# Kernel optimization log

Measured on AMD Instinct MI355X. Metric: run time of the kernel, lower is better.

Reference implementation:

```python
import jax, jax.numpy as jnp
import numpy as np

NUM_RELS = 1000
NFEATS = 128
RFEATS = 64
B = 32768
P = 1  # norm order


def setup_inputs() -> dict:
    key = jax.random.key(0)
    k1, k2, k3, k4, k5 = jax.random.split(key, 5)
    h_head = jax.random.normal(k1, (B, NFEATS), dtype=jnp.float32)
    h_tail = jax.random.normal(k2, (B, NFEATS), dtype=jnp.float32)
    rels = jax.random.randint(k3, (B,), 0, NUM_RELS, dtype=jnp.int64)
    rel_emb_table = jax.random.normal(k4, (NUM_RELS, RFEATS), dtype=jnp.float32)
    rel_project_table = jax.random.normal(k5, (NUM_RELS, NFEATS * RFEATS), dtype=jnp.float32)
    return {
        "h_head": h_head,
        "h_tail": h_tail,
        "rels": rels,
        "rel_emb_table": rel_emb_table,
        "rel_project_table": rel_project_table,
    }


def reference(h_head, h_tail, rels, rel_emb_table, rel_project_table):
    # per-relation gathers
    h_rel = rel_emb_table[rels]                                    # [B, rfeats]
    proj_rel = rel_project_table[rels].reshape(-1, NFEATS, RFEATS)  # [B, nfeats, rfeats]
    # batched vector-matrix projection of head/tail into relation space
    ph = jnp.einsum("bn,bnr->br", h_head, proj_rel)               # [B, rfeats]
    pt = jnp.einsum("bn,bnr->br", h_tail, proj_rel)               # [B, rfeats]
    diff = ph + h_rel - pt                                         # [B, rfeats]
    # p=1 norm along last dim, negated score
    return -jnp.sum(jnp.abs(diff), axis=-1)                        # [B]
```

## Files before the change

kernel.cpp:

```cpp
#include <hip/hip_runtime.h>


#define NFEATS   128
#define RFEATS   64
#define NUM_RELS 1000
#define STRIDE   128

#define AS_GLOBAL __attribute__((address_space(1)))
#define AS_SHARED __attribute__((address_space(3)))

__global__ void scatter_kernel(const int* __restrict__ rels,
                               int* __restrict__ cursors,
                               int* __restrict__ bucket, int B) {
    int i = blockIdx.x * blockDim.x + threadIdx.x;
    if (i < B) {
        int r = rels[i];
        int s = atomicAdd(&cursors[r], 1);
        if (s < STRIDE) bucket[(r << 7) + s] = i;
    }
}

__global__ __launch_bounds__(512, 8) void transr_main(
    const float* __restrict__ h_head,
    const float* __restrict__ h_tail,
    const float* __restrict__ rel_emb,
    const float* __restrict__ rel_proj,
    const int*   __restrict__ cursors,
    const int*   __restrict__ bucket,
    float* __restrict__ out)
{
    __shared__ float Plds[NFEATS * RFEATS];

    const int r    = blockIdx.x;
    const int tid  = threadIdx.x;
    const int w    = tid >> 6;
    const int lane = tid & 63;

    const float* Psrc = rel_proj + (size_t)r * (NFEATS * RFEATS);
#if __has_builtin(__builtin_amdgcn_global_load_lds)
#pragma unroll
    for (int it = 0; it < 4; ++it) {
        const int off = (it * 512 + tid) * 4;
        __builtin_amdgcn_global_load_lds(
            (const AS_GLOBAL void*)(Psrc + off),
            (AS_SHARED void*)(Plds + off), 16, 0, 0);
    }
#else
#pragma unroll
    for (int it = 0; it < 4; ++it) {
        const int off = (it * 512 + tid) * 4;
        *(float4*)(Plds + off) = *(const float4*)(Psrc + off);
    }
#endif

    int cnt = cursors[r];
    if (cnt > STRIDE) cnt = STRIDE;

    const float ev = rel_emb[(size_t)r * RFEATS + lane];
    const int* buk = bucket + (r << 7);

    int    rowid[4];
    float2 d2[4];
#pragma unroll
    for (int rr = 0; rr < 4; ++rr) {
        const int li = w * 4 + rr;
        rowid[rr] = (li < cnt) ? buk[li] : -1;
        d2[rr] = make_float2(0.f, 0.f);
        if (rowid[rr] >= 0) {
            const float2 a = *(const float2*)(h_head + (size_t)rowid[rr] * NFEATS + lane * 2);
            const float2 b = *(const float2*)(h_tail + (size_t)rowid[rr] * NFEATS + lane * 2);
            d2[rr].x = a.x - b.x;
            d2[rr].y = a.y - b.y;
        }
    }

    __syncthreads();

    for (int base = 0; base < cnt; base += 32) {
        if (base + w * 4 < cnt) {
            float acc0 = 0.f, acc1 = 0.f, acc2 = 0.f, acc3 = 0.f;

#pragma unroll 8
            for (int q = 0; q < 64; ++q) {
                const float p0 = Plds[(2 * q) * RFEATS + lane];
                const float p1 = Plds[(2 * q + 1) * RFEATS + lane];

                float dx, dy;
                dx = __uint_as_float(__builtin_amdgcn_readlane(__float_as_uint(d2[0].x), q));
                dy = __uint_as_float(__builtin_amdgcn_readlane(__float_as_uint(d2[0].y), q));
                acc0 = fmaf(dx, p0, acc0); acc0 = fmaf(dy, p1, acc0);
                dx = __uint_as_float(__builtin_amdgcn_readlane(__float_as_uint(d2[1].x), q));
                dy = __uint_as_float(__builtin_amdgcn_readlane(__float_as_uint(d2[1].y), q));
                acc1 = fmaf(dx, p0, acc1); acc1 = fmaf(dy, p1, acc1);
                dx = __uint_as_float(__builtin_amdgcn_readlane(__float_as_uint(d2[2].x), q));
                dy = __uint_as_float(__builtin_amdgcn_readlane(__float_as_uint(d2[2].y), q));
                acc2 = fmaf(dx, p0, acc2); acc2 = fmaf(dy, p1, acc2);
                dx = __uint_as_float(__builtin_amdgcn_readlane(__float_as_uint(d2[3].x), q));
                dy = __uint_as_float(__builtin_amdgcn_readlane(__float_as_uint(d2[3].y), q));
                acc3 = fmaf(dx, p0, acc3); acc3 = fmaf(dy, p1, acc3);
            }

            float s[4] = { fabsf(acc0 + ev), fabsf(acc1 + ev),
                           fabsf(acc2 + ev), fabsf(acc3 + ev) };
#pragma unroll
            for (int rr = 0; rr < 4; ++rr) {
                float sv = s[rr];
                sv += __shfl_xor(sv, 1);
                sv += __shfl_xor(sv, 2);
                sv += __shfl_xor(sv, 4);
                sv += __shfl_xor(sv, 8);
                sv += __shfl_xor(sv, 16);
                sv += __shfl_xor(sv, 32);
                if (lane == rr && rowid[rr] >= 0) out[rowid[rr]] = -sv;
            }
        }

        const int nbase = base + 32;
        if (nbase < cnt) {
#pragma unroll
            for (int rr = 0; rr < 4; ++rr) {
                const int li = nbase + w * 4 + rr;
                rowid[rr] = (li < cnt) ? buk[li] : -1;
                d2[rr] = make_float2(0.f, 0.f);
                if (rowid[rr] >= 0) {
                    const float2 a = *(const float2*)(h_head + (size_t)rowid[rr] * NFEATS + lane * 2);
                    const float2 b = *(const float2*)(h_tail + (size_t)rowid[rr] * NFEATS + lane * 2);
                    d2[rr].x = a.x - b.x;
                    d2[rr].y = a.y - b.y;
                }
            }
        }
    }
}

extern "C" void kernel_launch(void* const* d_in, const int* in_sizes, int n_in,
                              void* d_out, int out_size, void* d_ws, size_t ws_size,
                              hipStream_t stream) {
    const float* h_head   = (const float*)d_in[0];
    const float* h_tail   = (const float*)d_in[1];
    const int*   rels     = (const int*)d_in[2];
    const float* rel_emb  = (const float*)d_in[3];
    const float* rel_proj = (const float*)d_in[4];
    float* out = (float*)d_out;

    const int B = in_sizes[2];

    int* cursors = (int*)d_ws;
    int* bucket  = cursors + 1024;

    hipMemsetAsync(cursors, 0, 1024 * sizeof(int), stream);
    scatter_kernel<<<(B + 255) / 256, 256, 0, stream>>>(rels, cursors, bucket, B);
    transr_main<<<NUM_RELS, 512, 0, stream>>>(h_head, h_tail, rel_emb, rel_proj,
                                              cursors, bucket, out);
}
```

Measured before the change: 134.9 us.

## Stage head-tail difference in LDS and pipeline projection loads with compute

Each warp now writes its head-minus-tail rows into a shared Dlds buffer instead of broadcasting them with readlane. Each lane computes four output columns from float4 reads of the projection matrix, over a split of the feature dimension, and a two-stage xor shuffle combines the partial sums. The first 32-row chunk waits on the async global-to-LDS loads in four parts with staged vmcnt waits, so computation begins before the whole matrix has arrived. Occupancy is lowered to six blocks to allow the larger LDS footprint. Blocks with no rows now exit early. The row loop that runs past the first chunk writes Dlds again without a barrier, which is safe only because each warp touches only its own rows.

```diff
diff --git a/kernel.cpp b/kernel.cpp
--- a/kernel.cpp
+++ b/kernel.cpp
@@ -20,7 +20,28 @@
     }
 }
 
-__global__ __launch_bounds__(512, 8) void transr_main(
+__device__ __forceinline__ void reduce_store(const float acc[4][4],
+                                             const int rowid[4],
+                                             float4 e4, int lane,
+                                             float* __restrict__ out) {
+#pragma unroll
+    for (int rr = 0; rr < 4; ++rr) {
+        float a0 = acc[rr][0], a1 = acc[rr][1], a2 = acc[rr][2], a3 = acc[rr][3];
+        a0 += __shfl_xor(a0, 20); a0 += __shfl_xor(a0, 40);
+        a1 += __shfl_xor(a1, 20); a1 += __shfl_xor(a1, 40);
+        a2 += __shfl_xor(a2, 20); a2 += __shfl_xor(a2, 40);
+        a3 += __shfl_xor(a3, 20); a3 += __shfl_xor(a3, 40);
+        float sv = fabsf(a0 + e4.x) + fabsf(a1 + e4.y)
+                 + fabsf(a2 + e4.z) + fabsf(a3 + e4.w);
+        sv += __shfl_xor(sv, 1);
+        sv += __shfl_xor(sv, 2);
+        sv += __shfl_xor(sv, 4);
+        sv += __shfl_xor(sv, 8);
+        if (lane == rr && rowid[rr] >= 0) out[rowid[rr]] = -sv;
+    }
+}
+
+__global__ __launch_bounds__(512, 6) void transr_main(
     const float* __restrict__ h_head,
     const float* __restrict__ h_tail,
     const float* __restrict__ rel_emb,
@@ -30,105 +51,124 @@
     float* __restrict__ out)
 {
     __shared__ float Plds[NFEATS * RFEATS];
+    __shared__ float Dlds[32][NFEATS];
 
     const int r    = blockIdx.x;
     const int tid  = threadIdx.x;
     const int w    = tid >> 6;
     const int lane = tid & 63;
+    const int jg   = lane & 15;
+    const int p    = lane >> 4;
+    const int cq   = jg ^ (p << 2);
+
+    int cnt = cursors[r];
+    if (cnt > STRIDE) cnt = STRIDE;
+    if (cnt == 0) return;
+
+    const int* buk = bucket + (r << 7);
+
+    int rowid[4];
+#pragma unroll
+    for (int rr = 0; rr < 4; ++rr) {
+        const int li  = (w << 2) + rr;
+        const int row = (li < cnt) ? buk[li] : -1;
+        rowid[rr] = row;
+        float2 d = make_float2(0.f, 0.f);
+        if (row >= 0) {
+            const float2 a = *(const float2*)(h_head + (size_t)row * NFEATS + (lane << 1));
+            const float2 b = *(const float2*)(h_tail + (size_t)row * NFEATS + (lane << 1));
+            d.x = a.x - b.x;
+            d.y = a.y - b.y;
+        }
+        *(float2*)(&Dlds[(w << 2) + rr][lane << 1]) = d;
+    }
 
     const float* Psrc = rel_proj + (size_t)r * (NFEATS * RFEATS);
-#if __has_builtin(__builtin_amdgcn_global_load_lds)
 #pragma unroll
     for (int it = 0; it < 4; ++it) {
         const int off = (it * 512 + tid) * 4;
-        __builtin_amdgcn_global_load_lds(
-            (const AS_GLOBAL void*)(Psrc + off),
-            (AS_SHARED void*)(Plds + off), 16, 0, 0);
+        __builtin_amdgcn_global_load_lds((const AS_GLOBAL void*)(Psrc + off),
+                                         (AS_SHARED void*)(Plds + off), 16, 0, 0);
     }
-#else
-#pragma unroll
-    for (int it = 0; it < 4; ++it) {
-        const int off = (it * 512 + tid) * 4;
-        *(float4*)(Plds + off) = *(const float4*)(Psrc + off);
-    }
-#endif
+    __builtin_amdgcn_sched_barrier(0);
 
-    int cnt = cursors[r];
-    if (cnt > STRIDE) cnt = STRIDE;
-
-    const float ev = rel_emb[(size_t)r * RFEATS + lane];
-    const int* buk = bucket + (r << 7);
-
-    int    rowid[4];
-    float2 d2[4];
+    float acc[4][4];
 #pragma unroll
     for (int rr = 0; rr < 4; ++rr) {
-        const int li = w * 4 + rr;
-        rowid[rr] = (li < cnt) ? buk[li] : -1;
-        d2[rr] = make_float2(0.f, 0.f);
-        if (rowid[rr] >= 0) {
-            const float2 a = *(const float2*)(h_head + (size_t)rowid[rr] * NFEATS + lane * 2);
-            const float2 b = *(const float2*)(h_tail + (size_t)rowid[rr] * NFEATS + lane * 2);
-            d2[rr].x = a.x - b.x;
-            d2[rr].y = a.y - b.y;
+        acc[rr][0] = 0.f; acc[rr][1] = 0.f; acc[rr][2] = 0.f; acc[rr][3] = 0.f;
+    }
+
+    const char*  Pb   = (const char*)Plds;
+    const int    pcq  = (p << 8) | (cq << 4);
+    const float* drow = &Dlds[w << 2][p];
+    bool havework = ((w << 2) < cnt);
+
+#pragma unroll
+    for (int s = 0; s < 4; ++s) {
+        if      (s == 0) asm volatile("s_waitcnt vmcnt(3)" ::: "memory");
+        else if (s == 1) asm volatile("s_waitcnt vmcnt(2)" ::: "memory");
+        else if (s == 2) asm volatile("s_waitcnt vmcnt(1)" ::: "memory");
+        else             asm volatile("s_waitcnt vmcnt(0)" ::: "memory");
+        __builtin_amdgcn_sched_barrier(0);
+        __builtin_amdgcn_s_barrier();
+        if (havework) {
+#pragma unroll
+            for (int t = 0; t < 8; ++t) {
+                const float4 pv = *(const float4*)(Pb + s * 8192 + t * 1024 + pcq);
+#pragma unroll
+                for (int rr = 0; rr < 4; ++rr) {
+                    const float dv = drow[rr * 128 + s * 32 + t * 4];
+                    acc[rr][0] = fmaf(dv, pv.x, acc[rr][0]);
+                    acc[rr][1] = fmaf(dv, pv.y, acc[rr][1]);
+                    acc[rr][2] = fmaf(dv, pv.z, acc[rr][2]);
+                    acc[rr][3] = fmaf(dv, pv.w, acc[rr][3]);
+                }
+            }
         }
     }
 
-    __syncthreads();
+    const float4 e4 = *(const float4*)(rel_emb + (size_t)r * RFEATS + (cq << 2));
 
-    for (int base = 0; base < cnt; base += 32) {
-        if (base + w * 4 < cnt) {
-            float acc0 = 0.f, acc1 = 0.f, acc2 = 0.f, acc3 = 0.f;
+    if (havework) reduce_store(acc, rowid, e4, lane, out);
 
-#pragma unroll 8
-            for (int q = 0; q < 64; ++q) {
-                const float p0 = Plds[(2 * q) * RFEATS + lane];
-                const float p1 = Plds[(2 * q + 1) * RFEATS + lane];
+    for (int base = 32; base < cnt; base += 32) {
+#pragma unroll
+        for (int rr = 0; rr < 4; ++rr) {
+            const int li  = base + (w << 2) + rr;
+            const int row = (li < cnt) ? buk[li] : -1;
+            rowid[rr] = row;
+            float2 d = make_float2(0.f, 0.f);
+            if (row >= 0) {
+                const float2 a = *(const float2*)(h_head + (size_t)row * NFEATS + (lane << 1));
+                const float2 b = *(const float2*)(h_tail + (size_t)row * NFEATS + (lane << 1));
+                d.x = a.x - b.x;
+                d.y = a.y - b.y;
+            }
+            *(float2*)(&Dlds[(w << 2) + rr][lane << 1]) = d;
+        }
 
-                float dx, dy;
-                dx = __uint_as_float(__builtin_amdgcn_readlane(__float_as_uint(d2[0].x), q));
-                dy = __uint_as_float(__builtin_amdgcn_readlane(__float_as_uint(d2[0].y), q));
-                acc0 = fmaf(dx, p0, acc0); acc0 = fmaf(dy, p1, acc0);
-                dx = __uint_as_float(__builtin_amdgcn_readlane(__float_as_uint(d2[1].x), q));
-                dy = __uint_as_float(__builtin_amdgcn_readlane(__float_as_uint(d2[1].y), q));
-                acc1 = fmaf(dx, p0, acc1); acc1 = fmaf(dy, p1, acc1);
-                dx = __uint_as_float(__builtin_amdgcn_readlane(__float_as_uint(d2[2].x), q));
-                dy = __uint_as_float(__builtin_amdgcn_readlane(__float_as_uint(d2[2].y), q));
-                acc2 = fmaf(dx, p0, acc2); acc2 = fmaf(dy, p1, acc2);
-                dx = __uint_as_float(__builtin_amdgcn_readlane(__float_as_uint(d2[3].x), q));
-                dy = __uint_as_float(__builtin_amdgcn_readlane(__float_as_uint(d2[3].y), q));
-                acc3 = fmaf(dx, p0, acc3); acc3 = fmaf(dy, p1, acc3);
-            }
-
-            float s[4] = { fabsf(acc0 + ev), fabsf(acc1 + ev),
-                           fabsf(acc2 + ev), fabsf(acc3 + ev) };
+        havework = (base + (w << 2) < cnt);
+        if (havework) {
 #pragma unroll
             for (int rr = 0; rr < 4; ++rr) {
-                float sv = s[rr];
-                sv += __shfl_xor(sv, 1);
-                sv += __shfl_xor(sv, 2);
-                sv += __shfl_xor(sv, 4);
-                sv += __shfl_xor(sv, 8);
-                sv += __shfl_xor(sv, 16);
-                sv += __shfl_xor(sv, 32);
-                if (lane == rr && rowid[rr] >= 0) out[rowid[rr]] = -sv;
+                acc[rr][0] = 0.f; acc[rr][1] = 0.f; acc[rr][2] = 0.f; acc[rr][3] = 0.f;
             }
-        }
-
-        const int nbase = base + 32;
-        if (nbase < cnt) {
 #pragma unroll
-            for (int rr = 0; rr < 4; ++rr) {
-                const int li = nbase + w * 4 + rr;
-                rowid[rr] = (li < cnt) ? buk[li] : -1;
-                d2[rr] = make_float2(0.f, 0.f);
-                if (rowid[rr] >= 0) {
-                    const float2 a = *(const float2*)(h_head + (size_t)rowid[rr] * NFEATS + lane * 2);
-                    const float2 b = *(const float2*)(h_tail + (size_t)rowid[rr] * NFEATS + lane * 2);
-                    d2[rr].x = a.x - b.x;
-                    d2[rr].y = a.y - b.y;
+            for (int s = 0; s < 4; ++s) {
+#pragma unroll
+                for (int t = 0; t < 8; ++t) {
+                    const float4 pv = *(const float4*)(Pb + s * 8192 + t * 1024 + pcq);
+#pragma unroll
+                    for (int rr = 0; rr < 4; ++rr) {
+                        const float dv = drow[rr * 128 + s * 32 + t * 4];
+                        acc[rr][0] = fmaf(dv, pv.x, acc[rr][0]);
+                        acc[rr][1] = fmaf(dv, pv.y, acc[rr][1]);
+                        acc[rr][2] = fmaf(dv, pv.z, acc[rr][2]);
+                        acc[rr][3] = fmaf(dv, pv.w, acc[rr][3]);
+                    }
                 }
             }
+            reduce_store(acc, rowid, e4, lane, out);
         }
     }
 }
```

After: 215.2 us. +59.5%, slower.

## Process two relations per block with double-buffered LDS projection staging

Applied to the files above, without the earlier changes.

Each block now handles two relations, using two LDS buffers. The second relation's 32KB projection matrix is loaded asynchronously into LDS while the first relation's rows are computed, which hides global-to-LDS latency. In exchange the grid is halved to 500 blocks and LDS per block doubles to 64KB, which lowers occupancy and parallelism on a GPU with 256 CUs. There is also a possible hazard: the second buffer is written while the first is being read, though the two buffers are separate.

```diff
diff --git a/kernel.cpp b/kernel.cpp
--- a/kernel.cpp
+++ b/kernel.cpp
@@ -20,6 +20,72 @@
     }
 }
 
+
+#define STAGE(PBUF, RIDX)                                                      \
+    {                                                                          \
+        const float* Psrc_ = rel_proj + (size_t)(RIDX) * (NFEATS * RFEATS);    \
+        _Pragma("unroll")                                                      \
+        for (int it_ = 0; it_ < 4; ++it_) {                                    \
+            const int off_ = (it_ * 512 + tid) * 4;                            \
+            __builtin_amdgcn_global_load_lds(                                  \
+                (const AS_GLOBAL void*)(Psrc_ + off_),                         \
+                (AS_SHARED void*)((PBUF) + off_), 16, 0, 0);                   \
+        }                                                                      \
+    }
+
+#define LOADD(CNT, BUK, BASE)                                                  \
+    _Pragma("unroll")                                                          \
+    for (int rr_ = 0; rr_ < 4; ++rr_) {                                        \
+        const int li_ = (BASE) + (w << 2) + rr_;                               \
+        rowid[rr_] = (li_ < (CNT)) ? (BUK)[li_] : -1;                          \
+        d2[rr_] = make_float2(0.f, 0.f);                                       \
+        if (rowid[rr_] >= 0) {                                                 \
+            const float2 a_ = *(const float2*)(h_head + (size_t)rowid[rr_] * NFEATS + (lane << 1)); \
+            const float2 b_ = *(const float2*)(h_tail + (size_t)rowid[rr_] * NFEATS + (lane << 1)); \
+            d2[rr_].x = a_.x - b_.x;                                           \
+            d2[rr_].y = a_.y - b_.y;                                           \
+        }                                                                      \
+    }
+
+#define RL(dst, src, q) dst = __uint_as_float(__builtin_amdgcn_readlane(__float_as_uint(src), q))
+
+#define COMPUTE(CNT, BUK, PBUF, EV)                                            \
+    for (int base_ = 0; base_ < (CNT); base_ += 32) {                          \
+        if (base_ + (w << 2) < (CNT)) {                                        \
+            float acc0 = 0.f, acc1 = 0.f, acc2 = 0.f, acc3 = 0.f;              \
+            _Pragma("unroll 8")                                                \
+            for (int q = 0; q < 64; ++q) {                                     \
+                const float p0 = (PBUF)[(2 * q) * RFEATS + lane];              \
+                const float p1 = (PBUF)[(2 * q + 1) * RFEATS + lane];          \
+                float dx, dy;                                                  \
+                RL(dx, d2[0].x, q); RL(dy, d2[0].y, q);                        \
+                acc0 = fmaf(dx, p0, acc0); acc0 = fmaf(dy, p1, acc0);          \
+                RL(dx, d2[1].x, q); RL(dy, d2[1].y, q);                        \
+                acc1 = fmaf(dx, p0, acc1); acc1 = fmaf(dy, p1, acc1);          \
+                RL(dx, d2[2].x, q); RL(dy, d2[2].y, q);                        \
+                acc2 = fmaf(dx, p0, acc2); acc2 = fmaf(dy, p1, acc2);          \
+                RL(dx, d2[3].x, q); RL(dy, d2[3].y, q);                        \
+                acc3 = fmaf(dx, p0, acc3); acc3 = fmaf(dy, p1, acc3);          \
+            }                                                                  \
+            float s0 = fabsf(acc0 + (EV)), s1 = fabsf(acc1 + (EV));            \
+            float s2 = fabsf(acc2 + (EV)), s3 = fabsf(acc3 + (EV));            \
+            float sv_[4] = { s0, s1, s2, s3 };                                 \
+            _Pragma("unroll")                                                  \
+            for (int rr_ = 0; rr_ < 4; ++rr_) {                                \
+                float sv = sv_[rr_];                                           \
+                sv += __shfl_xor(sv, 1);                                       \
+                sv += __shfl_xor(sv, 2);                                       \
+                sv += __shfl_xor(sv, 4);                                       \
+                sv += __shfl_xor(sv, 8);                                       \
+                sv += __shfl_xor(sv, 16);                                      \
+                sv += __shfl_xor(sv, 32);                                      \
+                if (lane == rr_ && rowid[rr_] >= 0) out[rowid[rr_]] = -sv;     \
+            }                                                                  \
+        }                                                                      \
+        const int nb_ = base_ + 32;                                            \
+        if (nb_ < (CNT)) { LOADD((CNT), (BUK), nb_) }                          \
+    }
+
 __global__ __launch_bounds__(512, 8) void transr_main(
     const float* __restrict__ h_head,
     const float* __restrict__ h_tail,
@@ -29,108 +95,39 @@
     const int*   __restrict__ bucket,
     float* __restrict__ out)
 {
-    __shared__ float Plds[NFEATS * RFEATS];
+    __shared__ float Plds[2][NFEATS * RFEATS];
 
-    const int r    = blockIdx.x;
     const int tid  = threadIdx.x;
     const int w    = tid >> 6;
     const int lane = tid & 63;
 
-    const float* Psrc = rel_proj + (size_t)r * (NFEATS * RFEATS);
-#if __has_builtin(__builtin_amdgcn_global_load_lds)
-#pragma unroll
-    for (int it = 0; it < 4; ++it) {
-        const int off = (it * 512 + tid) * 4;
-        __builtin_amdgcn_global_load_lds(
-            (const AS_GLOBAL void*)(Psrc + off),
-            (AS_SHARED void*)(Plds + off), 16, 0, 0);
-    }
-#else
-#pragma unroll
-    for (int it = 0; it < 4; ++it) {
-        const int off = (it * 512 + tid) * 4;
-        *(float4*)(Plds + off) = *(const float4*)(Psrc + off);
-    }
-#endif
+    const int r0 = blockIdx.x << 1;
+    const int r1 = r0 + 1;
 
-    int cnt = cursors[r];
-    if (cnt > STRIDE) cnt = STRIDE;
+    STAGE(&Plds[0][0], r0)
 
-    const float ev = rel_emb[(size_t)r * RFEATS + lane];
-    const int* buk = bucket + (r << 7);
+    int cnt0 = cursors[r0]; if (cnt0 > STRIDE) cnt0 = STRIDE;
+    int cnt1 = cursors[r1]; if (cnt1 > STRIDE) cnt1 = STRIDE;
+    const int* buk0 = bucket + (r0 << 7);
+    const int* buk1 = bucket + (r1 << 7);
+    const float ev0 = rel_emb[(size_t)r0 * RFEATS + lane];
+    const float ev1 = rel_emb[(size_t)r1 * RFEATS + lane];
 
     int    rowid[4];
     float2 d2[4];
-#pragma unroll
-    for (int rr = 0; rr < 4; ++rr) {
-        const int li = w * 4 + rr;
-        rowid[rr] = (li < cnt) ? buk[li] : -1;
-        d2[rr] = make_float2(0.f, 0.f);
-        if (rowid[rr] >= 0) {
-            const float2 a = *(const float2*)(h_head + (size_t)rowid[rr] * NFEATS + lane * 2);
-            const float2 b = *(const float2*)(h_tail + (size_t)rowid[rr] * NFEATS + lane * 2);
-            d2[rr].x = a.x - b.x;
-            d2[rr].y = a.y - b.y;
-        }
-    }
+    LOADD(cnt0, buk0, 0)
 
     __syncthreads();
 
-    for (int base = 0; base < cnt; base += 32) {
-        if (base + w * 4 < cnt) {
-            float acc0 = 0.f, acc1 = 0.f, acc2 = 0.f, acc3 = 0.f;
+    STAGE(&Plds[1][0], r1)
 
-#pragma unroll 8
-            for (int q = 0; q < 64; ++q) {
-                const float p0 = Plds[(2 * q) * RFEATS + lane];
-                const float p1 = Plds[(2 * q + 1) * RFEATS + lane];
+    COMPUTE(cnt0, buk0, (&Plds[0][0]), ev0)
 
-                float dx, dy;
-                dx = __uint_as_float(__builtin_amdgcn_readlane(__float_as_uint(d2[0].x), q));
-                dy = __uint_as_float(__builtin_amdgcn_readlane(__float_as_uint(d2[0].y), q));
-                acc0 = fmaf(dx, p0, acc0); acc0 = fmaf(dy, p1, acc0);
-                dx = __uint_as_float(__builtin_amdgcn_readlane(__float_as_uint(d2[1].x), q));
-                dy = __uint_as_float(__builtin_amdgcn_readlane(__float_as_uint(d2[1].y), q));
-                acc1 = fmaf(dx, p0, acc1); acc1 = fmaf(dy, p1, acc1);
-                dx = __uint_as_float(__builtin_amdgcn_readlane(__float_as_uint(d2[2].x), q));
-                dy = __uint_as_float(__builtin_amdgcn_readlane(__float_as_uint(d2[2].y), q));
-                acc2 = fmaf(dx, p0, acc2); acc2 = fmaf(dy, p1, acc2);
-                dx = __uint_as_float(__builtin_amdgcn_readlane(__float_as_uint(d2[3].x), q));
-                dy = __uint_as_float(__builtin_amdgcn_readlane(__float_as_uint(d2[3].y), q));
-                acc3 = fmaf(dx, p0, acc3); acc3 = fmaf(dy, p1, acc3);
-            }
+    LOADD(cnt1, buk1, 0)
 
-            float s[4] = { fabsf(acc0 + ev), fabsf(acc1 + ev),
-                           fabsf(acc2 + ev), fabsf(acc3 + ev) };
-#pragma unroll
-            for (int rr = 0; rr < 4; ++rr) {
-                float sv = s[rr];
-                sv += __shfl_xor(sv, 1);
-                sv += __shfl_xor(sv, 2);
-                sv += __shfl_xor(sv, 4);
-                sv += __shfl_xor(sv, 8);
-                sv += __shfl_xor(sv, 16);
-                sv += __shfl_xor(sv, 32);
-                if (lane == rr && rowid[rr] >= 0) out[rowid[rr]] = -sv;
-            }
-        }
+    __syncthreads();
 
-        const int nbase = base + 32;
-        if (nbase < cnt) {
-#pragma unroll
-            for (int rr = 0; rr < 4; ++rr) {
-                const int li = nbase + w * 4 + rr;
-                rowid[rr] = (li < cnt) ? buk[li] : -1;
-                d2[rr] = make_float2(0.f, 0.f);
-                if (rowid[rr] >= 0) {
-                    const float2 a = *(const float2*)(h_head + (size_t)rowid[rr] * NFEATS + lane * 2);
-                    const float2 b = *(const float2*)(h_tail + (size_t)rowid[rr] * NFEATS + lane * 2);
-                    d2[rr].x = a.x - b.x;
-                    d2[rr].y = a.y - b.y;
-                }
-            }
-        }
-    }
+    COMPUTE(cnt1, buk1, (&Plds[1][0]), ev1)
 }
 
 extern "C" void kernel_launch(void* const* d_in, const int* in_sizes, int n_in,
@@ -150,6 +147,6 @@
 
     hipMemsetAsync(cursors, 0, 1024 * sizeof(int), stream);
     scatter_kernel<<<(B + 255) / 256, 256, 0, stream>>>(rels, cursors, bucket, B);
-    transr_main<<<NUM_RELS, 512, 0, stream>>>(h_head, h_tail, rel_emb, rel_proj,
-                                              cursors, bucket, out);
+    transr_main<<<NUM_RELS / 2, 512, 0, stream>>>(h_head, h_tail, rel_emb, rel_proj,
+                                                  cursors, bucket, out);
 }
```

Measured after the change: 139.9 us. +3.7%, slower.
